# Performance work log

Measured on AMD Instinct MI355X. Metric: run time of the kernel, lower is better.

The kernel has to match this reference:

```python
import jax, jax.numpy as jnp
import numpy as np

EPS = 1e-6

def setup_inputs() -> dict:
    key = jax.random.key(0)
    k1, k2, k3, k4, k5 = jax.random.split(key, 5)
    nb, ngrid, ntarget, nbasis, nchannel = 8, 512, 1024, 5, 3
    x_grid = jax.random.normal(k1, (nb, ngrid, nchannel), dtype=jnp.float32)
    h_grid = jax.random.normal(k2, (nb, ngrid, nbasis, nchannel), dtype=jnp.float32)
    target_x = jax.random.normal(k3, (nb, ntarget, nchannel), dtype=jnp.float32)
    # sigma = log(min_init + init_length_scale * ones) per module init
    sigma = jnp.log(1e-6 + 1.0 * jnp.ones((nbasis, nchannel), dtype=jnp.float32))
    g_w = jax.random.normal(k4, (1, nbasis), dtype=jnp.float32) / jnp.sqrt(nbasis)
    g_b = jnp.zeros((1,), dtype=jnp.float32)
    return {"x_grid": x_grid, "h_grid": h_grid, "target_x": target_x,
            "sigma": sigma, "g_w": g_w, "g_b": g_b}

def reference(x_grid, h_grid, target_x, sigma, g_w, g_b):
    # scales: (nbasis, nchannel)
    scales = jnp.exp(sigma) + EPS
    # pairwise diffs: (b, ngrid, ntarget, 1, c) -> broadcast over nbasis
    d = (x_grid[:, :, None, None, :] - target_x[:, None, :, None, :]) / scales
    wt = jnp.exp(-0.5 * d * d)  # (b, g, t, k, c)
    # weighted sum over grid: h_grid (b, g, k, c)
    h_out = jnp.einsum('bgkc,bgtkc->btkc', h_grid, wt)  # (b, t, k, c)
    h_out = jnp.swapaxes(h_out, -2, -1)  # (b, t, c, k)
    out = jnp.einsum('btck,ok->btco', h_out, g_w) + g_b  # (b, t, c, 1)
    return jnp.squeeze(out, axis=-1)  # (b, t, c)
```

## Files before the change

### kernel.cpp

```cpp
#include <hip/hip_runtime.h>

#define NB 8
#define NG 512
#define NT 1024
#define NK 5
#define NC 3
#define TT 8
#define TW 2

#define HALF_LOG2E 0.72134752044448170f

#if defined(__has_builtin)
#if __has_builtin(__builtin_amdgcn_exp2f)
#define EXP2F(x) __builtin_amdgcn_exp2f(x)
#else
#define EXP2F(x) exp2f(x)
#endif
#else
#define EXP2F(x) exp2f(x)
#endif

__global__ __launch_bounds__(256)
void fused_kernel(const float* __restrict__ x_grid,
                  const float* __restrict__ h_grid,
                  const float* __restrict__ target_x,
                  const float* __restrict__ sigma,
                  const float* __restrict__ g_w,
                  const float* __restrict__ g_b,
                  float* __restrict__ out) {
    __shared__ float xb_s[NC][NG];
    __shared__ float hs_s[NC][NG];

    const int tid   = threadIdx.x;
    const int b     = blockIdx.x / (NT / TT);
    const int ttile = blockIdx.x % (NT / TT);
    const int wave  = tid >> 6;
    const int lane  = tid & 63;
    const int t0    = ttile * TT + wave * TW;

    float sig0[NC];
    #pragma unroll
    for (int c = 0; c < NC; ++c) sig0[c] = sigma[c];
    bool kuni = true;
    #pragma unroll
    for (int k = 1; k < NK; ++k)
        #pragma unroll
        for (int c = 0; c < NC; ++c)
            kuni = kuni && (sigma[k * NC + c] == sig0[c]);

    float acc[TW][NC] = {};

    if (kuni) {
        float beta[NC];
        #pragma unroll
        for (int c = 0; c < NC; ++c) {
            float s = __expf(sig0[c]) + 1e-6f;
            beta[c] = sqrtf(HALF_LOG2E) / s;
        }
        float gw[NK];
        #pragma unroll
        for (int k = 0; k < NK; ++k) gw[k] = g_w[k];

        {
            const float* __restrict__ hp = h_grid + (size_t)b * NG * NK * NC + tid * 2 * NK * NC;
            const float* __restrict__ xp = x_grid + (size_t)b * NG * NC + tid * 2 * NC;
            #pragma unroll
            for (int gg = 0; gg < 2; ++gg) {
                const int g = tid * 2 + gg;
                float hs[NC] = {};
                #pragma unroll
                for (int k = 0; k < NK; ++k)
                    #pragma unroll
                    for (int c = 0; c < NC; ++c)
                        hs[c] += gw[k] * hp[gg * NK * NC + k * NC + c];
                #pragma unroll
                for (int c = 0; c < NC; ++c) {
                    hs_s[c][g] = hs[c];
                    xb_s[c][g] = xp[gg * NC + c] * beta[c];
                }
            }
        }

        float tb[TW][NC];
        #pragma unroll
        for (int t = 0; t < TW; ++t)
            #pragma unroll
            for (int c = 0; c < NC; ++c)
                tb[t][c] = target_x[((size_t)b * NT + t0 + t) * NC + c] * beta[c];

        __syncthreads();

        #pragma unroll
        for (int i = 0; i < NG / 64; ++i) {
            const int g = lane + i * 64;
            float xv[NC], hv[NC];
            #pragma unroll
            for (int c = 0; c < NC; ++c) {
                xv[c] = xb_s[c][g];
                hv[c] = hs_s[c][g];
            }
            #pragma unroll
            for (int t = 0; t < TW; ++t) {
                #pragma unroll
                for (int c = 0; c < NC; ++c) {
                    float a = xv[c] - tb[t][c];
                    acc[t][c] += hv[c] * EXP2F(-(a * a));
                }
            }
        }
    } else {
        float gw[NK], coef[NK][NC], txr[TW][NC];
        #pragma unroll
        for (int k = 0; k < NK; ++k) gw[k] = g_w[k];
        #pragma unroll
        for (int k = 0; k < NK; ++k)
            #pragma unroll
            for (int c = 0; c < NC; ++c) {
                float s = __expf(sigma[k * NC + c]) + 1e-6f;
                coef[k][c] = -HALF_LOG2E / (s * s);
            }
        #pragma unroll
        for (int t = 0; t < TW; ++t)
            #pragma unroll
            for (int c = 0; c < NC; ++c)
                txr[t][c] = target_x[((size_t)b * NT + t0 + t) * NC + c];

        #pragma unroll 1
        for (int i = 0; i < NG / 64; ++i) {
            const int g = lane + i * 64;
            float xv[NC];
            #pragma unroll
            for (int c = 0; c < NC; ++c)
                xv[c] = x_grid[((size_t)b * NG + g) * NC + c];
            float hv[NK][NC];
            #pragma unroll
            for (int k = 0; k < NK; ++k)
                #pragma unroll
                for (int c = 0; c < NC; ++c)
                    hv[k][c] = gw[k] * h_grid[(((size_t)b * NG + g) * NK + k) * NC + c];
            #pragma unroll
            for (int t = 0; t < TW; ++t) {
                float d2[NC];
                #pragma unroll
                for (int c = 0; c < NC; ++c) {
                    float d = xv[c] - txr[t][c];
                    d2[c] = d * d;
                }
                #pragma unroll
                for (int k = 0; k < NK; ++k)
                    #pragma unroll
                    for (int c = 0; c < NC; ++c)
                        acc[t][c] += hv[k][c] * EXP2F(d2[c] * coef[k][c]);
            }
        }
    }

    #pragma unroll
    for (int t = 0; t < TW; ++t)
        #pragma unroll
        for (int c = 0; c < NC; ++c) {
            float v = acc[t][c];
            #pragma unroll
            for (int off = 32; off > 0; off >>= 1)
                v += __shfl_down(v, off);
            acc[t][c] = v;
        }

    if (lane == 0) {
        const float gb = g_b[0];
        #pragma unroll
        for (int t = 0; t < TW; ++t)
            #pragma unroll
            for (int c = 0; c < NC; ++c)
                out[((size_t)b * NT + t0 + t) * NC + c] = acc[t][c] + gb;
    }
}

extern "C" void kernel_launch(void* const* d_in, const int* in_sizes, int n_in,
                              void* d_out, int out_size, void* d_ws, size_t ws_size,
                              hipStream_t stream) {
    const float* x_grid   = (const float*)d_in[0];
    const float* h_grid   = (const float*)d_in[1];
    const float* target_x = (const float*)d_in[2];
    const float* sigma    = (const float*)d_in[3];
    const float* g_w      = (const float*)d_in[4];
    const float* g_b      = (const float*)d_in[5];
    float* out = (float*)d_out;

    const int grid = NB * (NT / TT);
    fused_kernel<<<grid, 256, 0, stream>>>(x_grid, h_grid, target_x,
                                           sigma, g_w, g_b, out);
}
```

Before: 11.00 us.

## Widen target tile per wave, pack LDS as float4, use DPP wave reduction

```diff
diff --git a/kernel.cpp b/kernel.cpp
--- a/kernel.cpp
+++ b/kernel.cpp
@@ -5,8 +5,8 @@
 #define NT 1024
 #define NK 5
 #define NC 3
-#define TT 8
-#define TW 2
+#define TT 32
+#define TW 8
 
 #define HALF_LOG2E 0.72134752044448170f
 
@@ -20,6 +20,21 @@
 #define EXP2F(x) exp2f(x)
 #endif
 
+template <int CTRL>
+__device__ __forceinline__ float dpp_add(float v) {
+    int x = __builtin_amdgcn_update_dpp(0, __float_as_int(v), CTRL, 0xf, 0xf, true);
+    return v + __int_as_float(x);
+}
+__device__ __forceinline__ float wave_sum_lane63(float v) {
+    v = dpp_add<0x111>(v);
+    v = dpp_add<0x112>(v);
+    v = dpp_add<0x114>(v);
+    v = dpp_add<0x118>(v);
+    v = dpp_add<0x142>(v);
+    v = dpp_add<0x143>(v);
+    return v;
+}
+
 __global__ __launch_bounds__(256)
 void fused_kernel(const float* __restrict__ x_grid,
                   const float* __restrict__ h_grid,
@@ -28,8 +43,8 @@
                   const float* __restrict__ g_w,
                   const float* __restrict__ g_b,
                   float* __restrict__ out) {
-    __shared__ float xb_s[NC][NG];
-    __shared__ float hs_s[NC][NG];
+    __shared__ float4 xb_s[NG];
+    __shared__ float4 hs_s[NG];
 
     const int tid   = threadIdx.x;
     const int b     = blockIdx.x / (NT / TT);
@@ -48,8 +63,6 @@
         for (int c = 0; c < NC; ++c)
             kuni = kuni && (sigma[k * NC + c] == sig0[c]);
 
-    float acc[TW][NC] = {};
-
     if (kuni) {
         float beta[NC];
         #pragma unroll
@@ -73,11 +86,10 @@
                     #pragma unroll
                     for (int c = 0; c < NC; ++c)
                         hs[c] += gw[k] * hp[gg * NK * NC + k * NC + c];
-                #pragma unroll
-                for (int c = 0; c < NC; ++c) {
-                    hs_s[c][g] = hs[c];
-                    xb_s[c][g] = xp[gg * NC + c] * beta[c];
-                }
+                hs_s[g] = make_float4(hs[0], hs[1], hs[2], 0.f);
+                xb_s[g] = make_float4(xp[gg * NC + 0] * beta[0],
+                                      xp[gg * NC + 1] * beta[1],
+                                      xp[gg * NC + 2] * beta[2], 0.f);
             }
         }
 
@@ -90,23 +102,37 @@
 
         __syncthreads();
 
-        #pragma unroll
+        float acc[TW][NC] = {};
+
+        #pragma unroll 2
         for (int i = 0; i < NG / 64; ++i) {
             const int g = lane + i * 64;
-            float xv[NC], hv[NC];
-            #pragma unroll
-            for (int c = 0; c < NC; ++c) {
-                xv[c] = xb_s[c][g];
-                hv[c] = hs_s[c][g];
-            }
+            const float4 xv = xb_s[g];
+            const float4 hv = hs_s[g];
             #pragma unroll
             for (int t = 0; t < TW; ++t) {
-                #pragma unroll
-                for (int c = 0; c < NC; ++c) {
-                    float a = xv[c] - tb[t][c];
-                    acc[t][c] += hv[c] * EXP2F(-(a * a));
-                }
-            }
+                float a0 = xv.x - tb[t][0];
+                float a1 = xv.y - tb[t][1];
+                float a2 = xv.z - tb[t][2];
+                acc[t][0] += hv.x * EXP2F(-(a0 * a0));
+                acc[t][1] += hv.y * EXP2F(-(a1 * a1));
+                acc[t][2] += hv.z * EXP2F(-(a2 * a2));
+            }
+        }
+
+        #pragma unroll
+        for (int t = 0; t < TW; ++t)
+            #pragma unroll
+            for (int c = 0; c < NC; ++c)
+                acc[t][c] = wave_sum_lane63(acc[t][c]);
+
+        if (lane == 63) {
+            const float gb = g_b[0];
+            #pragma unroll
+            for (int t = 0; t < TW; ++t)
+                #pragma unroll
+                for (int c = 0; c < NC; ++c)
+                    out[((size_t)b * NT + t0 + t) * NC + c] = acc[t][c] + gb;
         }
     } else {
         float gw[NK], coef[NK][NC], txr[TW][NC];
@@ -124,6 +150,8 @@
             #pragma unroll
             for (int c = 0; c < NC; ++c)
                 txr[t][c] = target_x[((size_t)b * NT + t0 + t) * NC + c];
+
+        float acc[TW][NC] = {};
 
         #pragma unroll 1
         for (int i = 0; i < NG / 64; ++i) {
@@ -153,26 +181,21 @@
                         acc[t][c] += hv[k][c] * EXP2F(d2[c] * coef[k][c]);
             }
         }
-    }
-
-    #pragma unroll
-    for (int t = 0; t < TW; ++t)
-        #pragma unroll
-        for (int c = 0; c < NC; ++c) {
-            float v = acc[t][c];
-            #pragma unroll
-            for (int off = 32; off > 0; off >>= 1)
-                v += __shfl_down(v, off);
-            acc[t][c] = v;
-        }
-
-    if (lane == 0) {
-        const float gb = g_b[0];
-        #pragma unroll
-        for (int t = 0; t < TW; ++t)
-            #pragma unroll
-            for (int c = 0; c < NC; ++c)
-                out[((size_t)b * NT + t0 + t) * NC + c] = acc[t][c] + gb;
+
+        #pragma unroll
+        for (int t = 0; t < TW; ++t)
+            #pragma unroll
+            for (int c = 0; c < NC; ++c)
+                acc[t][c] = wave_sum_lane63(acc[t][c]);
+
+        if (lane == 63) {
+            const float gb = g_b[0];
+            #pragma unroll
+            for (int t = 0; t < TW; ++t)
+                #pragma unroll
+                for (int c = 0; c < NC; ++c)
+                    out[((size_t)b * NT + t0 + t) * NC + c] = acc[t][c] + gb;
+        }
     }
 }
 
```

New measurement: 10.51 us. 4.5% less time.
